# Optimization experiments

Measured on AMD Instinct MI355X. Metric: run time of the kernel, lower is better.

Reference implementation:

```python
import jax, jax.numpy as jnp
import numpy as np
import math

B, S, D, DC, H, L = 8, 4096, 1024, 1024, 16, 2
TOPK, TEMP, MAX_DEPTH, EPS = 2, 1.0, 32, 1e-5

def _gelu(x):
    return jax.nn.gelu(x, approximate=False)

def _ln(x, g=None, b=None):
    mu = x.mean(-1, keepdims=True)
    xc = x - mu
    var = (xc * xc).mean(-1, keepdims=True)
    y = xc * jax.lax.rsqrt(var + EPS)
    if g is not None:
        y = y * g + b
    return y

def setup_inputs() -> dict:
    key = jax.random.key(0)
    ks = iter(jax.random.split(key, 40))
    w = lambda *sh: jax.random.normal(next(ks), sh, dtype=jnp.float32) * 0.02
    inp = {}
    inp['X'] = jax.random.normal(next(ks), (B, S, D), dtype=jnp.float32)
    inp['z'] = jax.random.normal(next(ks), (B, DC), dtype=jnp.float32)
    inp['step_idx'] = 3
    # pool LayerNorm (affine) + input projection
    inp['g_pool'] = jnp.ones((D,)); inp['b_pool'] = jnp.zeros((D,))
    inp['W_inp'] = w(D, DC); inp['b_inp'] = jnp.zeros((DC,))
    # timestep embedding MLP
    inp['Wt1'] = w(DC, 4 * DC); inp['bt1'] = jnp.zeros((4 * DC,))
    inp['Wt2'] = w(4 * DC, DC); inp['bt2'] = jnp.zeros((DC,))
    # cond fusion
    inp['Wc1'] = w(2 * DC, DC); inp['bc1'] = jnp.zeros((DC,))
    inp['Wc2'] = w(DC, DC); inp['bc2'] = jnp.zeros((DC,))
    # denoise blocks (stacked over L)
    inp['W_mod'] = w(L, DC, 4 * DC); inp['b_mod'] = jnp.zeros((L, 4 * DC))
    inp['Wm1'] = w(L, DC, 4 * DC); inp['bm1'] = jnp.zeros((L, 4 * DC))
    inp['Wm2'] = w(L, 4 * DC, DC); inp['bm2'] = jnp.zeros((L, DC))
    # final proj + ln_z
    inp['Wf'] = w(DC, DC); inp['bf'] = jnp.zeros((DC,))
    inp['gz'] = jnp.ones((DC,)); inp['bz'] = jnp.zeros((DC,))
    # router: LN(D+DC) -> Linear -> GELU -> Linear(H)
    inp['gr'] = jnp.ones((D + DC,)); inp['br'] = jnp.zeros((D + DC,))
    inp['Wr1'] = w(D + DC, DC); inp['br1'] = jnp.zeros((DC,))
    inp['Wr2'] = w(DC, H); inp['br2'] = jnp.zeros((H,))
    return inp

def _forward(X, z, step_idx, g_pool, b_pool, W_inp, b_inp, Wt1, bt1, Wt2, bt2,
             Wc1, bc1, Wc2, bc2, W_mod, b_mod, Wm1, bm1, Wm2, bm2,
             Wf, bf, gz, bz, gr, br, Wr1, br1, Wr2, br2):
    # pool tokens -> control vector
    g = _ln(X, g_pool, b_pool).mean(axis=1)            # [B, D]
    x_ctrl = g @ W_inp + b_inp                          # [B, DC]
    # cosine noise schedule, sigma at this depth step
    t = jnp.linspace(0.0, 1.0, MAX_DEPTH)
    sigma_sched = jnp.clip(jnp.cos(t * (math.pi / 2)), 1e-4, None)
    sig = sigma_sched[min(int(step_idx), MAX_DEPTH - 1)]
    # sinusoidal timestep embedding + MLP
    half = DC // 2
    freqs = jnp.exp(-math.log(10000.0) * jnp.arange(half, dtype=jnp.float32) / half)
    args = jnp.broadcast_to(sig * freqs, (B, half))
    emb = jnp.concatenate([jnp.cos(args), jnp.sin(args)], axis=-1)  # [B, DC]
    t_embed = _gelu(emb @ Wt1 + bt1) @ Wt2 + bt2
    # conditioning fusion
    cond = jnp.concatenate([x_ctrl, t_embed], axis=-1)
    cond = _gelu(cond @ Wc1 + bc1) @ Wc2 + bc2          # [B, DC]
    # adaLN denoise blocks
    z_cur = z
    for l in range(L):
        mod = _gelu(cond) @ W_mod[l] + b_mod[l]
        s1, sh1, s2, sh2 = jnp.split(mod, 4, axis=-1)
        h = _ln(z_cur) * (1.0 + s1) + sh1
        h = _gelu(h @ Wm1[l] + bm1[l]) @ Wm2[l] + bm2[l]
        h = h * (1.0 + s2) + sh2
        z_cur = z_cur + h
    z_cur = z_cur @ Wf + bf
    z_cur = _ln(z_cur, gz, bz)                          # [B, DC]
    # token-conditioned router
    zt = jnp.broadcast_to(z_cur[:, None, :], (B, S, DC))
    r = _ln(jnp.concatenate([X, zt], axis=-1), gr, br)  # [B, S, D+DC]
    logits = _gelu(r @ Wr1 + br1) @ Wr2 + br2           # [B, S, H]
    alpha = jax.nn.softmax(logits / TEMP, axis=-1)
    # top-k mask + renormalize
    topv, topi = jax.lax.top_k(alpha, TOPK)
    bi = jnp.arange(B)[:, None, None]
    si = jnp.arange(S)[None, :, None]
    masked = jnp.zeros_like(alpha).at[bi, si, topi].set(topv)
    denom = jnp.maximum(masked.sum(axis=-1, keepdims=True), 1e-12)
    return masked / denom                               # [B, S, H]

def reference(X, z, step_idx, g_pool, b_pool, W_inp, b_inp, Wt1, bt1, Wt2, bt2,
              Wc1, bc1, Wc2, bc2, W_mod, b_mod, Wm1, bm1, Wm2, bm2,
              Wf, bf, gz, bz, gr, br, Wr1, br1, Wr2, br2):
    return _forward(X, z, step_idx, g_pool, b_pool, W_inp, b_inp, Wt1, bt1, Wt2, bt2,
                    Wc1, bc1, Wc2, bc2, W_mod, b_mod, Wm1, bm1, Wm2, bm2,
                    Wf, bf, gz, bz, gr, br, Wr1, br1, Wr2, br2)
```

## Files before the change

kernel.cpp:

```cpp
#include <hip/hip_runtime.h>
#include <cstdint>
#include <cstddef>
#include <math.h>

#define DEV __device__ __forceinline__


typedef short s8v __attribute__((ext_vector_type(8)));
typedef float f4v __attribute__((ext_vector_type(4)));

DEV float geluf(float x) { return 0.5f * x * (1.0f + erff(x * 0.70710678118654752440f)); }
DEV double gelud(double x) { return 0.5 * x * (1.0 + erf(x * 0.70710678118654752440)); }
DEV unsigned short f2us(float f) {
    unsigned u = __float_as_uint(f);
    u += 0x7fffu + ((u >> 16) & 1u);
    return (unsigned short)(u >> 16);
}

DEV void gload16(const void* g, void* l) {
    __builtin_amdgcn_global_load_lds(
        (const __attribute__((address_space(1))) void*)g,
        (__attribute__((address_space(3))) void*)l, 16, 0, 0);
}

DEV void blockReduce2d(double& a, double& b, double* lds ) {
    __syncthreads();
#pragma unroll
    for (int off = 32; off >= 1; off >>= 1) {
        a += __shfl_xor(a, off, 64);
        b += __shfl_xor(b, off, 64);
    }
    int w = threadIdx.x >> 6;
    if ((threadIdx.x & 63) == 0) { lds[w] = a; lds[4 + w] = b; }
    __syncthreads();
    a = lds[0] + lds[1] + lds[2] + lds[3];
    b = lds[4] + lds[5] + lds[6] + lds[7];
    __syncthreads();
}

__global__ __launch_bounds__(256) void pool_kernel(
    const float* __restrict__ X, double* __restrict__ Macc,
    double* __restrict__ tokstats)
{
    int b = blockIdx.y;
    int w = threadIdx.x >> 6, l = threadIdx.x & 63;
    int s0 = blockIdx.x * 64 + w * 16;
    double acc[16];
#pragma unroll
    for (int e = 0; e < 16; e++) acc[e] = 0.0;
    __shared__ double red[4][1024];

    for (int t = 0; t < 16; t++) {
        int s = s0 + t;
        const float* row = X + (size_t)(b * 4096 + s) * 1024;
        float xv[16];
#pragma unroll
        for (int m = 0; m < 16; m++) xv[m] = row[l + 64 * m];
        double s1 = 0.0, s2 = 0.0;
#pragma unroll
        for (int m = 0; m < 16; m++) { double x = (double)xv[m]; s1 += x; s2 += x * x; }
#pragma unroll
        for (int off = 32; off >= 1; off >>= 1) {
            s1 += __shfl_xor(s1, off, 64);
            s2 += __shfl_xor(s2, off, 64);
        }
        double mu = s1 * (1.0 / 1024.0);
        double var = s2 * (1.0 / 1024.0) - mu * mu;
        double istd = 1.0 / sqrt(var + 1e-5);
        if (l == 0) {
            tokstats[(size_t)(b * 4096 + s) * 2]     = s1;
            tokstats[(size_t)(b * 4096 + s) * 2 + 1] = s2;
        }
#pragma unroll
        for (int m = 0; m < 16; m++) acc[m] += ((double)xv[m] - mu) * istd;
    }
#pragma unroll
    for (int m = 0; m < 16; m++) red[w][l + 64 * m] = acc[m];
    __syncthreads();
    for (int d = threadIdx.x; d < 1024; d += 256)
        atomicAdd(&Macc[b * 1024 + d], red[0][d] + red[1][d] + red[2][d] + red[3][d]);
}

__global__ void prep_kernel(const int* __restrict__ step_idx,
                            const float* __restrict__ z,
                            double* __restrict__ emb, double* __restrict__ z0)
{
    int step = step_idx[0];
    if (step > 31) step = 31;
    double t = (double)step / 31.0;
    double sig = cos(t * 1.5707963267948966);
    if (sig < 1e-4) sig = 1e-4;
    for (int k = threadIdx.x; k < 512; k += 256) {
        double fr = exp(-9.210340371976184 * ((double)k / 512.0));
        double a = sig * fr;
        emb[k] = cos(a);
        emb[512 + k] = sin(a);
    }
    for (int i = threadIdx.x; i < 8192; i += 256) z0[i] = (double)z[i];
}

__global__ __launch_bounds__(256) void prepw_kernel(
    const float* __restrict__ Wr1, const float* __restrict__ gr,
    unsigned short* __restrict__ WThi, unsigned short* __restrict__ WTlo)
{
    __shared__ unsigned short th[64][65], tl[64][65];
    int tx = threadIdx.x & 63, ty = threadIdx.x >> 6;
    int i0 = blockIdx.y * 64, j0 = blockIdx.x * 64;
#pragma unroll 4
    for (int k = 0; k < 16; k++) {
        int row = ty * 16 + k;
        float w = (float)((double)gr[i0 + row] * (double)Wr1[(size_t)(i0 + row) * 1024 + j0 + tx]);
        unsigned short hi = f2us(w);
        float hif = __uint_as_float((unsigned)hi << 16);
        unsigned short lo = f2us(w - hif);
        th[row][tx] = hi;
        tl[row][tx] = lo;
    }
    __syncthreads();
#pragma unroll 4
    for (int k = 0; k < 16; k++) {
        int row = ty * 16 + k;
        WThi[(size_t)(j0 + row) * 1024 + i0 + tx] = th[tx][row];
        WTlo[(size_t)(j0 + row) * 1024 + i0 + tx] = tl[tx][row];
    }
}

__global__ __launch_bounds__(256) void colsum_kernel(
    const float* __restrict__ Wr1, const float* __restrict__ gr,
    const float* __restrict__ br, const float* __restrict__ br1,
    double* __restrict__ Cvec, double* __restrict__ hbvec)
{
    int j = blockIdx.x * 256 + threadIdx.x;
    double c = 0.0, bw = 0.0;
    for (int i = 0; i < 2048; i++) {
        double wv = (double)Wr1[(size_t)i * 1024 + j];
        c += (double)gr[i] * wv;
        bw += (double)br[i] * wv;
    }
    Cvec[j] = c;
    hbvec[j] = bw + (double)br1[j];
}

template <int IN, int R>
__global__ __launch_bounds__(256) void gemvd_kernel(
    const float* __restrict__ W, int K, int N, int kchunk, int kstr,
    const double* __restrict__ in0, const double* __restrict__ in1,
    const double* __restrict__ in2,
    const float* __restrict__ ba0, const float* __restrict__ ba1,
    double* __restrict__ out)
{
    const int CH = 64;
    __shared__ double xin[R][CH];
    int tid = threadIdx.x;
    int j = blockIdx.x * 256 + tid;
    int kbeg = blockIdx.y * kchunk;
    double acc[R];
#pragma unroll
    for (int r = 0; r < R; r++) acc[r] = 0.0;

    for (int k0 = kbeg; k0 < kbeg + kchunk; k0 += CH) {
        for (int idx = tid; idx < R * CH; idx += 256) {
            int r = idx / CH, ii = idx % CH, i = k0 + ii;
            double v;
            if (IN == 0) {
                v = in0[(size_t)r * kstr + i] + (ba0 ? (double)ba0[i] : 0.0);
            } else if (IN == 1) {
                v = (double)ba0[i] * (in0[(size_t)r * kstr + i] * (1.0 / 4096.0)) + (double)ba1[i];
            } else if (IN == 2) {
                v = gelud(in0[(size_t)r * kstr + i] + (ba0 ? (double)ba0[i] : 0.0));
            } else if (IN == 3) {
                double mu = in1[r * 2], istd = in1[r * 2 + 1];
                double s1 = in2[(size_t)r * 4096 + i] + (double)ba0[i];
                double sh1 = in2[(size_t)r * 4096 + 1024 + i] + (double)ba0[1024 + i];
                v = (in0[(size_t)r * 1024 + i] - mu) * istd * (1.0 + s1) + sh1;
            } else {
                v = (i < 1024) ? (in0[(size_t)r * 1024 + i] + (double)ba0[i])
                               : (in1[i - 1024] + (double)ba1[i - 1024]);
            }
            xin[r][ii] = v;
        }
        __syncthreads();
#pragma unroll 16
        for (int kk = 0; kk < CH; kk++) {
            double wv = (double)W[(size_t)(k0 + kk) * N + j];
#pragma unroll
            for (int r = 0; r < R; r++) acc[r] += xin[r][kk] * wv;
        }
        __syncthreads();
    }
#pragma unroll
    for (int r = 0; r < R; r++) atomicAdd(&out[(size_t)r * N + j], acc[r]);
}

__global__ void stats8_kernel(const double* __restrict__ z, double* __restrict__ zstats)
{
    __shared__ double lds[8];
    int r = blockIdx.x, tid = threadIdx.x;
    double s = 0.0, ss = 0.0;
    for (int i = tid; i < 1024; i += 256) {
        double v = z[(size_t)r * 1024 + i];
        s += v; ss += v * v;
    }
    blockReduce2d(s, ss, lds);
    if (tid == 0) {
        double mu = s * (1.0 / 1024.0);
        double var = ss * (1.0 / 1024.0) - mu * mu;
        zstats[r * 2] = mu;
        zstats[r * 2 + 1] = 1.0 / sqrt(var + 1e-5);
    }
}

__global__ void resid_kernel(const double* __restrict__ zc, const double* __restrict__ h2pre,
                             const float* __restrict__ bm2,
                             const double* __restrict__ modpre,
                             const float* __restrict__ bmod,
                             double* __restrict__ znew, double* __restrict__ zstats)
{
    __shared__ double lds[8];
    int r = blockIdx.x, tid = threadIdx.x;
    double s = 0.0, ss = 0.0;
#pragma unroll
    for (int c = 0; c < 4; c++) {
        int i = tid + c * 256;
        double s2 = modpre[(size_t)r * 4096 + 2048 + i] + (double)bmod[2048 + i];
        double sh2 = modpre[(size_t)r * 4096 + 3072 + i] + (double)bmod[3072 + i];
        double h = h2pre[(size_t)r * 1024 + i] + (double)bm2[i];
        double v = zc[(size_t)r * 1024 + i] + h * (1.0 + s2) + sh2;
        znew[(size_t)r * 1024 + i] = v;
        s += v; ss += v * v;
    }
    blockReduce2d(s, ss, lds);
    if (tid == 0) {
        double mu = s * (1.0 / 1024.0);
        double var = ss * (1.0 / 1024.0) - mu * mu;
        zstats[r * 2] = mu;
        zstats[r * 2 + 1] = 1.0 / sqrt(var + 1e-5);
    }
}

__global__ void zfinal_kernel(const double* __restrict__ zfpre,
                              const float* __restrict__ bfb,
                              const float* __restrict__ gz,
                              const float* __restrict__ bz,
                              const float* __restrict__ gr,
                              double* __restrict__ zv, double* __restrict__ zrstats)
{
    __shared__ double xb[1024];
    __shared__ double lds[8];
    int r = blockIdx.x, tid = threadIdx.x;
    double s = 0.0, ss = 0.0;
#pragma unroll
    for (int c = 0; c < 4; c++) {
        int i = tid + c * 256;
        double x = zfpre[(size_t)r * 1024 + i] + (double)bfb[i];
        xb[i] = x;
        s += x; ss += x * x;
    }
    blockReduce2d(s, ss, lds);
    double mu = s * (1.0 / 1024.0);
    double var = ss * (1.0 / 1024.0) - mu * mu;
    double istd = 1.0 / sqrt(var + 1e-5);
    double s2 = 0.0, s2s = 0.0;
#pragma unroll
    for (int c = 0; c < 4; c++) {
        int i = tid + c * 256;
        double zf = (xb[i] - mu) * istd * (double)gz[i] + (double)bz[i];
        zv[(size_t)r * 1024 + i] = zf * (double)gr[1024 + i];
        s2 += zf; s2s += zf * zf;
    }
    blockReduce2d(s2, s2s, lds);
    if (tid == 0) { zrstats[r * 2] = s2; zrstats[r * 2 + 1] = s2s; }
}

__global__ __launch_bounds__(256) void router_kernel(
    const float* __restrict__ X, const unsigned short* __restrict__ WThi,
    const unsigned short* __restrict__ WTlo,
    const double* __restrict__ tokstats, const double* __restrict__ zrstats,
    const double* __restrict__ Vmat, const double* __restrict__ Cvec,
    const double* __restrict__ hbvec, const float* __restrict__ Wr2,
    float* __restrict__ logits)
{
    __shared__ struct {
        union {
            struct { float Af[128 * 32]; unsigned short Bh[128 * 32]; unsigned short Bl[128 * 32]; } g;
            struct { float Ht[64 * 133]; float W2[1024]; } e;
        } u;
        float mus[128], iss[128], Vs[128], Cs[128], hbs[128];
    } sm;

    const int tid = threadIdx.x;
    const int n0 = blockIdx.x * 128, tok0 = blockIdx.y * 128;
    const int b = tok0 >> 12;

    if (tid < 128) {
        int tok = tok0 + tid;
        double mu = (tokstats[(size_t)tok * 2] + zrstats[b * 2]) * (1.0 / 2048.0);
        double var = (tokstats[(size_t)tok * 2 + 1] + zrstats[b * 2 + 1]) * (1.0 / 2048.0) - mu * mu;
        sm.mus[tid] = (float)mu;
        sm.iss[tid] = (float)(1.0 / sqrt(var + 1e-5));
    } else {
        int n = tid - 128;
        sm.Vs[n] = (float)Vmat[(size_t)b * 1024 + n0 + n];
        sm.Cs[n] = (float)Cvec[n0 + n];
        sm.hbs[n] = (float)hbvec[n0 + n];
    }

    const int l = tid & 63, wid = tid >> 6;
    const int wm = wid >> 1, wn = wid & 1;
    const int lr = l & 15, q = l >> 4;

    const float* gA[4]; char* lA[4];
#pragma unroll
    for (int it = 0; it < 4; it++) {
        int c = it * 256 + tid;
        int m = c >> 3;
        int pg = (c & 7) ^ (m & 7);
        gA[it] = X + (size_t)(tok0 + m) * 1024 + pg * 4;
        lA[it] = (char*)sm.u.g.Af + c * 16;
    }
    const unsigned short *gBh[2], *gBl[2];
    char *lBh[2], *lBl[2];
#pragma unroll
    for (int it = 0; it < 2; it++) {
        int c = it * 256 + tid;
        int m = c >> 2;
        int p = (c & 3) ^ ((m >> 1) & 3);
        gBh[it] = WThi + (size_t)(n0 + m) * 1024 + p * 8;
        gBl[it] = WTlo + (size_t)(n0 + m) * 1024 + p * 8;
        lBh[it] = (char*)sm.u.g.Bh + c * 16;
        lBl[it] = (char*)sm.u.g.Bl + c * 16;
    }

    int boff[4], aoffr[4], s7a[4];
#pragma unroll
    for (int i = 0; i < 4; i++) {
        int rb = wn * 64 + i * 16 + lr;
        boff[i] = rb * 32 + ((q ^ ((rb >> 1) & 3)) << 3);
        int ra = wm * 64 + i * 16 + lr;
        aoffr[i] = ra * 32;
        s7a[i] = ra & 7;
    }

    f4v acc[4][4];
#pragma unroll
    for (int mi = 0; mi < 4; mi++)
#pragma unroll
        for (int ni = 0; ni < 4; ni++) acc[mi][ni] = (f4v){0.f, 0.f, 0.f, 0.f};

    for (int k0 = 0; k0 < 1024; k0 += 32) {
#pragma unroll
        for (int it = 0; it < 4; it++) gload16(gA[it] + k0, lA[it]);
#pragma unroll
        for (int it = 0; it < 2; it++) {
            gload16(gBh[it] + k0, lBh[it]);
            gload16(gBl[it] + k0, lBl[it]);
        }
        __syncthreads();

        s8v ah[4], al[4], bh4[4], bl4[4];
#pragma unroll
        for (int i = 0; i < 4; i++) {
            const float* Ab = sm.u.g.Af + aoffr[i];
            float4 f0 = *(const float4*)(Ab + ((((2 * q))     ^ s7a[i]) << 2));
            float4 f1 = *(const float4*)(Ab + ((((2 * q) | 1) ^ s7a[i]) << 2));
            unsigned u0 = __float_as_uint(f0.x), u1 = __float_as_uint(f0.y),
                     u2 = __float_as_uint(f0.z), u3 = __float_as_uint(f0.w),
                     u4 = __float_as_uint(f1.x), u5 = __float_as_uint(f1.y),
                     u6 = __float_as_uint(f1.z), u7 = __float_as_uint(f1.w);
            int4 hi4, lo4;
            hi4.x = (int)((u0 >> 16) | (u1 & 0xffff0000u));
            hi4.y = (int)((u2 >> 16) | (u3 & 0xffff0000u));
            hi4.z = (int)((u4 >> 16) | (u5 & 0xffff0000u));
            hi4.w = (int)((u6 >> 16) | (u7 & 0xffff0000u));
            float r0 = f0.x - __uint_as_float(u0 & 0xffff0000u);
            float r1 = f0.y - __uint_as_float(u1 & 0xffff0000u);
            float r2 = f0.z - __uint_as_float(u2 & 0xffff0000u);
            float r3 = f0.w - __uint_as_float(u3 & 0xffff0000u);
            float r4 = f1.x - __uint_as_float(u4 & 0xffff0000u);
            float r5 = f1.y - __uint_as_float(u5 & 0xffff0000u);
            float r6 = f1.z - __uint_as_float(u6 & 0xffff0000u);
            float r7 = f1.w - __uint_as_float(u7 & 0xffff0000u);
            lo4.x = (int)((__float_as_uint(r0) >> 16) | (__float_as_uint(r1) & 0xffff0000u));
            lo4.y = (int)((__float_as_uint(r2) >> 16) | (__float_as_uint(r3) & 0xffff0000u));
            lo4.z = (int)((__float_as_uint(r4) >> 16) | (__float_as_uint(r5) & 0xffff0000u));
            lo4.w = (int)((__float_as_uint(r6) >> 16) | (__float_as_uint(r7) & 0xffff0000u));
            ah[i] = __builtin_bit_cast(s8v, hi4);
            al[i] = __builtin_bit_cast(s8v, lo4);
            bh4[i] = *(const s8v*)(sm.u.g.Bh + boff[i]);
            bl4[i] = *(const s8v*)(sm.u.g.Bl + boff[i]);
        }
#pragma unroll
        for (int mi = 0; mi < 4; mi++)
#pragma unroll
            for (int ni = 0; ni < 4; ni++) {
                acc[mi][ni] = __builtin_amdgcn_mfma_f32_16x16x32_bf16(ah[mi], bh4[ni], acc[mi][ni], 0, 0, 0);
                acc[mi][ni] = __builtin_amdgcn_mfma_f32_16x16x32_bf16(al[mi], bh4[ni], acc[mi][ni], 0, 0, 0);
                acc[mi][ni] = __builtin_amdgcn_mfma_f32_16x16x32_bf16(ah[mi], bl4[ni], acc[mi][ni], 0, 0, 0);
            }
        __syncthreads();
    }

    float lacc[8];
#pragma unroll
    for (int h = 0; h < 8; h++) lacc[h] = 0.f;
    const int g2 = tid >> 7, mrow = tid & 127;

#pragma unroll
    for (int p = 0; p < 2; p++) {
#pragma unroll
        for (int nh = 0; nh < 2; nh++) {
            int ni = 2 * p + nh;
            int n = wn * 64 + ni * 16 + lr;
            int jl = wn * 32 + nh * 16 + lr;
            float Vn = sm.Vs[n], Cn = sm.Cs[n], hbn = sm.hbs[n];
#pragma unroll
            for (int mi = 0; mi < 4; mi++) {
#pragma unroll
                for (int rr = 0; rr < 4; rr++) {
                    int m = wm * 64 + mi * 16 + q * 4 + rr;
                    float h = sm.iss[m] * (acc[mi][ni][rr] + Vn - sm.mus[m] * Cn) + hbn;
                    sm.u.e.Ht[jl * 133 + m] = geluf(h);
                }
            }
        }
        for (int idx = tid; idx < 1024; idx += 256) {
            int jl = idx >> 4;
            int n = ((jl >> 5) << 6) + p * 32 + (jl & 31);
            sm.u.e.W2[idx] = Wr2[(size_t)(n0 + n) * 16 + (idx & 15)];
        }
        __syncthreads();
#pragma unroll 8
        for (int jl = 0; jl < 64; jl++) {
            float x = sm.u.e.Ht[jl * 133 + mrow];
#pragma unroll
            for (int h = 0; h < 8; h++) lacc[h] += x * sm.u.e.W2[jl * 16 + g2 * 8 + h];
        }
        __syncthreads();
    }
#pragma unroll
    for (int h = 0; h < 8; h++)
        atomicAdd(&logits[(size_t)(tok0 + mrow) * 16 + g2 * 8 + h], lacc[h]);
}

#define FLAG_CAP 16384
__global__ __launch_bounds__(256) void softflag_kernel(
    const float* __restrict__ logits, const float* __restrict__ br2,
    float* __restrict__ out, int* __restrict__ cnt, int* __restrict__ flagged)
{
    int t = blockIdx.x * 256 + threadIdx.x;
    float v[16];
    const float4* lp = (const float4*)(logits + (size_t)t * 16);
    float4 a0 = lp[0], a1 = lp[1], a2 = lp[2], a3 = lp[3];
    v[0] = a0.x; v[1] = a0.y; v[2] = a0.z; v[3] = a0.w;
    v[4] = a1.x; v[5] = a1.y; v[6] = a1.z; v[7] = a1.w;
    v[8] = a2.x; v[9] = a2.y; v[10] = a2.z; v[11] = a2.w;
    v[12] = a3.x; v[13] = a3.y; v[14] = a3.z; v[15] = a3.w;
#pragma unroll
    for (int h = 0; h < 16; h++) v[h] += br2[h];
    int i1 = 0; float b1 = v[0];
#pragma unroll
    for (int h = 1; h < 16; h++) if (v[h] > b1) { b1 = v[h]; i1 = h; }
    int i2 = -1; float b2 = -3.4e38f;
#pragma unroll
    for (int h = 0; h < 16; h++) if (h != i1 && v[h] > b2) { b2 = v[h]; i2 = h; }
    float b3 = -3.4e38f;
#pragma unroll
    for (int h = 0; h < 16; h++) if (h != i1 && h != i2 && v[h] > b3) b3 = v[h];
    float mx = b1;
    float e1 = expf(b1 - mx), e2 = expf(b2 - mx);
    float s = 0.f;
#pragma unroll
    for (int h = 0; h < 16; h++) s += expf(v[h] - mx);
    float a1v = e1 / s, a2v = e2 / s;
    float den = fmaxf(a1v + a2v, 1e-12f);
    float r1 = a1v / den, r2 = a2v / den;
    float o[16];
#pragma unroll
    for (int h = 0; h < 16; h++) o[h] = (h == i1 ? r1 : (h == i2 ? r2 : 0.f));
    float4* op = (float4*)(out + (size_t)t * 16);
    op[0] = make_float4(o[0], o[1], o[2], o[3]);
    op[1] = make_float4(o[4], o[5], o[6], o[7]);
    op[2] = make_float4(o[8], o[9], o[10], o[11]);
    op[3] = make_float4(o[12], o[13], o[14], o[15]);
    if (b2 - b3 < 1e-3f) {
        int slot = atomicAdd(cnt, 1);
        if (slot < FLAG_CAP) flagged[slot] = t;
    }
}

__global__ void flagstat_kernel(const float* __restrict__ X,
                                const double* __restrict__ zrstats,
                                const int* __restrict__ cnt,
                                const int* __restrict__ flagged,
                                double* __restrict__ fstats)
{
    int n = cnt[0]; if (n > FLAG_CAP) n = FLAG_CAP;
    int s = blockIdx.x;
    if (s >= n) return;
    int tok = flagged[s], b = tok >> 12;
    int l = threadIdx.x;
    double s1 = 0.0, s2 = 0.0;
#pragma unroll
    for (int m = 0; m < 16; m++) {
        double x = (double)X[(size_t)tok * 1024 + l + 64 * m];
        s1 += x; s2 += x * x;
    }
#pragma unroll
    for (int off = 32; off >= 1; off >>= 1) {
        s1 += __shfl_xor(s1, off, 64);
        s2 += __shfl_xor(s2, off, 64);
    }
    if (l == 0) {
        double mu = (s1 + zrstats[b * 2]) * (1.0 / 2048.0);
        double var = (s2 + zrstats[b * 2 + 1]) * (1.0 / 2048.0) - mu * mu;
        fstats[s * 2] = mu;
        fstats[s * 2 + 1] = 1.0 / sqrt(var + 1e-5);
    }
}

__global__ __launch_bounds__(256) void exact2_kernel(
    const float* __restrict__ X, const float* __restrict__ Wr1,
    const float* __restrict__ gr, const double* __restrict__ zv,
    const double* __restrict__ Cvec, const double* __restrict__ hbvec,
    const float* __restrict__ Wr2,
    const int* __restrict__ cnt, const int* __restrict__ flagged,
    const double* __restrict__ fstats, double* __restrict__ exlog)
{
    int n = cnt[0]; if (n > FLAG_CAP) n = FLAG_CAP;
    const int c = blockIdx.y;
    if (c * 16 >= n) return;
    int nt = n - c * 16; if (nt > 16) nt = 16;

    __shared__ double aS[16][65];
    __shared__ double gS[16][129];
    __shared__ double mus[16], iss[16];
    __shared__ int toks[16];

    const int tid = threadIdx.x;
    const int j0 = blockIdx.x * 128;
    const int jl = tid & 127;
    const int j = j0 + jl;
    const int tg = (tid >> 7) * 8;

    if (tid < 16) {
        if (tid < nt) {
            toks[tid] = flagged[c * 16 + tid];
            mus[tid] = fstats[(size_t)(c * 16 + tid) * 2];
            iss[tid] = fstats[(size_t)(c * 16 + tid) * 2 + 1];
        } else {
            toks[tid] = 0; mus[tid] = 0.0; iss[tid] = 0.0;
        }
    }
    __syncthreads();

    double acc[8];
#pragma unroll
    for (int t = 0; t < 8; t++) acc[t] = 0.0;

    for (int i0 = 0; i0 < 2048; i0 += 64) {
        for (int idx = tid; idx < 1024; idx += 256) {
            int t = idx >> 6, ii = idx & 63, i = i0 + ii;
            double v = 0.0;
            if (t < nt) {
                int tok = toks[t];
                if (i < 1024)
                    v = (double)X[(size_t)tok * 1024 + i] * (double)gr[i];
                else
                    v = zv[(size_t)(tok >> 12) * 1024 + (i - 1024)];
            }
            aS[t][ii] = v;
        }
        __syncthreads();
#pragma unroll 8
        for (int ii = 0; ii < 64; ii++) {
            double wv = (double)Wr1[(size_t)(i0 + ii) * 1024 + j];
#pragma unroll
            for (int t = 0; t < 8; t++) acc[t] += aS[tg + t][ii] * wv;
        }
        __syncthreads();
    }

    {
        double Cj = Cvec[j], hbj = hbvec[j];
#pragma unroll
        for (int t = 0; t < 8; t++) {
            double pre = iss[tg + t] * (acc[t] - mus[tg + t] * Cj) + hbj;
            gS[tg + t][jl] = gelud(pre);
        }
    }
    __syncthreads();

    {
        int t = tid >> 4, h = tid & 15;
        double p = 0.0;
#pragma unroll 8
        for (int j2 = 0; j2 < 128; j2++)
            p += gS[t][j2] * (double)Wr2[(size_t)(j0 + j2) * 16 + h];
        if (t < nt)
            atomicAdd(&exlog[(size_t)(c * 16 + t) * 16 + h], p);
    }
}

__global__ __launch_bounds__(256) void fix_kernel(
    const double* __restrict__ exlog, const float* __restrict__ br2,
    const int* __restrict__ cnt, const int* __restrict__ flagged,
    float* __restrict__ out)
{
    int s = blockIdx.x * 256 + threadIdx.x;
    int n = cnt[0]; if (n > FLAG_CAP) n = FLAG_CAP;
    if (s >= n) return;
    int tok = flagged[s];
    double v[16];
#pragma unroll
    for (int h = 0; h < 16; h++) v[h] = exlog[(size_t)s * 16 + h] + (double)br2[h];
    int i1 = 0; double b1 = v[0];
#pragma unroll
    for (int h = 1; h < 16; h++) if (v[h] > b1) { b1 = v[h]; i1 = h; }
    int i2 = -1; double b2 = -1e300;
#pragma unroll
    for (int h = 0; h < 16; h++) if (h != i1 && v[h] > b2) { b2 = v[h]; i2 = h; }
    double ssum = 0.0;
#pragma unroll
    for (int h = 0; h < 16; h++) ssum += exp(v[h] - b1);
    double a1v = exp(b1 - b1) / ssum, a2v = exp(b2 - b1) / ssum;
    double den = a1v + a2v; if (den < 1e-12) den = 1e-12;
    float r1 = (float)(a1v / den), r2 = (float)(a2v / den);
#pragma unroll
    for (int h = 0; h < 16; h++)
        out[(size_t)tok * 16 + h] = (h == i1 ? r1 : (h == i2 ? r2 : 0.f));
}

extern "C" void kernel_launch(void* const* d_in, const int* in_sizes, int n_in,
                              void* d_out, int out_size, void* d_ws, size_t ws_size,
                              hipStream_t stream)
{
    const float* X      = (const float*)d_in[0];
    const float* z_in   = (const float*)d_in[1];
    const int*   stepi  = (const int*)d_in[2];
    const float* g_pool = (const float*)d_in[3];
    const float* b_pool = (const float*)d_in[4];
    const float* W_inp  = (const float*)d_in[5];
    const float* b_inp  = (const float*)d_in[6];
    const float* Wt1    = (const float*)d_in[7];
    const float* bt1    = (const float*)d_in[8];
    const float* Wt2    = (const float*)d_in[9];
    const float* bt2    = (const float*)d_in[10];
    const float* Wc1    = (const float*)d_in[11];
    const float* bc1    = (const float*)d_in[12];
    const float* Wc2    = (const float*)d_in[13];
    const float* bc2    = (const float*)d_in[14];
    const float* W_mod  = (const float*)d_in[15];
    const float* b_mod  = (const float*)d_in[16];
    const float* Wm1    = (const float*)d_in[17];
    const float* bm1    = (const float*)d_in[18];
    const float* Wm2    = (const float*)d_in[19];
    const float* bm2    = (const float*)d_in[20];
    const float* Wf     = (const float*)d_in[21];
    const float* bf_b   = (const float*)d_in[22];
    const float* gz     = (const float*)d_in[23];
    const float* bz     = (const float*)d_in[24];
    const float* gr     = (const float*)d_in[25];
    const float* br     = (const float*)d_in[26];
    const float* Wr1    = (const float*)d_in[27];
    const float* br1    = (const float*)d_in[28];
    const float* Wr2    = (const float*)d_in[29];
    const float* br2    = (const float*)d_in[30];

    char* wsb = (char*)d_ws;
    const size_t OB_LOGA  = 0;
    const size_t OB_EXLOG = 2097152;
    const size_t OB_CNT   = 4194304;
    const size_t OB_FLAG  = 4194368;
    const size_t OB_MACC  = 4259904;
    const size_t OB_XCTRL = 4325440;
    const size_t OB_TH1   = 4390976;
    const size_t OB_TEMB  = 4423744;
    const size_t OB_CH    = 4431936;
    const size_t OB_COND  = 4497472;
    const size_t OB_MOD   = 4563008;
    const size_t OB_H1    = 5087296;
    const size_t OB_H2    = 5611584;
    const size_t OB_ZFPRE = 5742656;
    const size_t OB_V     = 5808192;
    const size_t ZEND     = 5873728;
    const size_t OB_TOKST = 5873728;
    const size_t OB_FSTAT = 6398016;
    const size_t OB_EMB   = 6660160;
    const size_t OB_ZB0   = 6668352;
    const size_t OB_ZB1   = 6733888;
    const size_t OB_ZST   = 6799424;
    const size_t OB_ZRST  = 6799552;
    const size_t OB_ZV    = 6799680;
    const size_t OB_CVEC  = 6865216;
    const size_t OB_HB    = 6873408;
    const size_t OB_WTHI  = 6881600;
    const size_t OB_WTLO  = 8978752;

    unsigned short* WThi = (unsigned short*)(wsb + OB_WTHI);
    unsigned short* WTlo = (unsigned short*)(wsb + OB_WTLO);
    int* cntp  = (int*)(wsb + OB_CNT);
    int* flagp = (int*)(wsb + OB_FLAG);

    hipMemsetAsync(d_ws, 0, ZEND, stream);

    pool_kernel<<<dim3(64, 8), 256, 0, stream>>>(X, (double*)(wsb + OB_MACC), (double*)(wsb + OB_TOKST));
    prep_kernel<<<1, 256, 0, stream>>>(stepi, z_in, (double*)(wsb + OB_EMB), (double*)(wsb + OB_ZB0));
    prepw_kernel<<<dim3(16, 16), 256, 0, stream>>>(Wr1, gr, WThi, WTlo);
    colsum_kernel<<<4, 256, 0, stream>>>(Wr1, gr, br, br1, (double*)(wsb + OB_CVEC), (double*)(wsb + OB_HB));

    gemvd_kernel<1, 8><<<dim3(4, 16), 256, 0, stream>>>(W_inp, 1024, 1024, 64, 1024,
        (double*)(wsb + OB_MACC), nullptr, nullptr, g_pool, b_pool, (double*)(wsb + OB_XCTRL));
    gemvd_kernel<0, 1><<<dim3(16, 16), 256, 0, stream>>>(Wt1, 1024, 4096, 64, 1024,
        (double*)(wsb + OB_EMB), nullptr, nullptr, nullptr, nullptr, (double*)(wsb + OB_TH1));
    gemvd_kernel<2, 1><<<dim3(4, 16), 256, 0, stream>>>(Wt2, 4096, 1024, 256, 4096,
        (double*)(wsb + OB_TH1), nullptr, nullptr, bt1, nullptr, (double*)(wsb + OB_TEMB));
    gemvd_kernel<4, 8><<<dim3(4, 16), 256, 0, stream>>>(Wc1, 2048, 1024, 128, 1024,
        (double*)(wsb + OB_XCTRL), (double*)(wsb + OB_TEMB), nullptr, b_inp, bt2, (double*)(wsb + OB_CH));
    gemvd_kernel<2, 8><<<dim3(4, 16), 256, 0, stream>>>(Wc2, 1024, 1024, 64, 1024,
        (double*)(wsb + OB_CH), nullptr, nullptr, bc1, nullptr, (double*)(wsb + OB_COND));

    stats8_kernel<<<8, 256, 0, stream>>>((double*)(wsb + OB_ZB0), (double*)(wsb + OB_ZST));

    for (int ll = 0; ll < 2; ll++) {
        double* zcur  = (double*)(wsb + (ll == 0 ? OB_ZB0 : OB_ZB1));
        double* znext = (double*)(wsb + (ll == 0 ? OB_ZB1 : OB_ZB0));
        double* modp  = (double*)(wsb + OB_MOD) + (size_t)ll * 32768;
        double* h1p   = (double*)(wsb + OB_H1) + (size_t)ll * 32768;
        double* h2p   = (double*)(wsb + OB_H2) + (size_t)ll * 8192;
        gemvd_kernel<2, 8><<<dim3(16, 16), 256, 0, stream>>>(W_mod + (size_t)ll * 4194304,
            1024, 4096, 64, 1024, (double*)(wsb + OB_COND), nullptr, nullptr, bc2, nullptr, modp);
        gemvd_kernel<3, 8><<<dim3(16, 16), 256, 0, stream>>>(Wm1 + (size_t)ll * 4194304,
            1024, 4096, 64, 1024, zcur, (double*)(wsb + OB_ZST), modp, b_mod + ll * 4096, nullptr, h1p);
        gemvd_kernel<2, 8><<<dim3(4, 16), 256, 0, stream>>>(Wm2 + (size_t)ll * 4194304,
            4096, 1024, 256, 4096, h1p, nullptr, nullptr, bm1 + ll * 4096, nullptr, h2p);
        resid_kernel<<<8, 256, 0, stream>>>(zcur, h2p, bm2 + ll * 1024, modp,
                                            b_mod + ll * 4096, znext, (double*)(wsb + OB_ZST));
    }

    gemvd_kernel<0, 8><<<dim3(4, 16), 256, 0, stream>>>(Wf, 1024, 1024, 64, 1024,
        (double*)(wsb + OB_ZB0), nullptr, nullptr, nullptr, nullptr, (double*)(wsb + OB_ZFPRE));
    zfinal_kernel<<<8, 256, 0, stream>>>((double*)(wsb + OB_ZFPRE), bf_b, gz, bz, gr,
                                         (double*)(wsb + OB_ZV), (double*)(wsb + OB_ZRST));
    gemvd_kernel<0, 8><<<dim3(4, 16), 256, 0, stream>>>(Wr1 + (size_t)1024 * 1024,
        1024, 1024, 64, 1024, (double*)(wsb + OB_ZV), nullptr, nullptr, nullptr, nullptr,
        (double*)(wsb + OB_V));

    router_kernel<<<dim3(8, 256), 256, 0, stream>>>(X, WThi, WTlo,
        (double*)(wsb + OB_TOKST), (double*)(wsb + OB_ZRST), (double*)(wsb + OB_V),
        (double*)(wsb + OB_CVEC), (double*)(wsb + OB_HB), Wr2, (float*)(wsb + OB_LOGA));

    softflag_kernel<<<128, 256, 0, stream>>>((float*)(wsb + OB_LOGA), br2,
        (float*)d_out, cntp, flagp);
    flagstat_kernel<<<16384, 64, 0, stream>>>(X, (double*)(wsb + OB_ZRST), cntp, flagp,
        (double*)(wsb + OB_FSTAT));
    exact2_kernel<<<dim3(8, 1024), 256, 0, stream>>>(X, Wr1, gr, (double*)(wsb + OB_ZV),
        (double*)(wsb + OB_CVEC), (double*)(wsb + OB_HB), Wr2, cntp, flagp,
        (double*)(wsb + OB_FSTAT), (double*)(wsb + OB_EXLOG));
    fix_kernel<<<64, 256, 0, stream>>>((double*)(wsb + OB_EXLOG), br2, cntp, flagp,
        (float*)d_out);
}
```

Before: 1.810 ms.

## Pre-split X into bf16 hi/lo in pool pass and add MFMA router2 kernel

Measured after the change: 1.729 ms. -4.5%, faster.

```diff
diff --git a/kernel.cpp b/kernel.cpp
--- a/kernel.cpp
+++ b/kernel.cpp
@@ -40,7 +40,8 @@
 
 __global__ __launch_bounds__(256) void pool_kernel(
     const float* __restrict__ X, double* __restrict__ Macc,
-    double* __restrict__ tokstats)
+    double* __restrict__ tokstats,
+    unsigned short* __restrict__ XH, unsigned short* __restrict__ XL)
 {
     int b = blockIdx.y;
     int w = threadIdx.x >> 6, l = threadIdx.x & 63;
@@ -56,6 +57,16 @@
         float xv[16];
 #pragma unroll
         for (int m = 0; m < 16; m++) xv[m] = row[l + 64 * m];
+        if (XH) {
+            size_t base = (size_t)(b * 4096 + s) * 1024 + l;
+#pragma unroll
+            for (int m = 0; m < 16; m++) {
+                unsigned u = __float_as_uint(xv[m]);
+                XH[base + 64 * m] = (unsigned short)(u >> 16);
+                float r = xv[m] - __uint_as_float(u & 0xffff0000u);
+                XL[base + 64 * m] = (unsigned short)(__float_as_uint(r) >> 16);
+            }
+        }
         double s1 = 0.0, s2 = 0.0;
 #pragma unroll
         for (int m = 0; m < 16; m++) { double x = (double)xv[m]; s1 += x; s2 += x * x; }
@@ -131,14 +142,18 @@
     double* __restrict__ Cvec, double* __restrict__ hbvec)
 {
     int j = blockIdx.x * 256 + threadIdx.x;
+    int i0 = blockIdx.y * 128;
     double c = 0.0, bw = 0.0;
-    for (int i = 0; i < 2048; i++) {
+#pragma unroll 4
+    for (int k = 0; k < 128; k++) {
+        int i = i0 + k;
         double wv = (double)Wr1[(size_t)i * 1024 + j];
         c += (double)gr[i] * wv;
         bw += (double)br[i] * wv;
     }
-    Cvec[j] = c;
-    hbvec[j] = bw + (double)br1[j];
+    if (blockIdx.y == 0) bw += (double)br1[j];
+    atomicAdd(&Cvec[j], c);
+    atomicAdd(&hbvec[j], bw);
 }
 
 template <int IN, int R>
@@ -270,6 +285,147 @@
     }
     blockReduce2d(s2, s2s, lds);
     if (tid == 0) { zrstats[r * 2] = s2; zrstats[r * 2 + 1] = s2s; }
+}
+
+__global__ __launch_bounds__(256) void router2_kernel(
+    const unsigned short* __restrict__ XH, const unsigned short* __restrict__ XL,
+    const unsigned short* __restrict__ WThi, const unsigned short* __restrict__ WTlo,
+    const double* __restrict__ tokstats, const double* __restrict__ zrstats,
+    const double* __restrict__ Vmat, const double* __restrict__ Cvec,
+    const double* __restrict__ hbvec, const float* __restrict__ Wr2,
+    float* __restrict__ logits)
+{
+    __shared__ struct {
+        union {
+            struct { unsigned short Ah[128 * 32], Al[128 * 32],
+                                    Bh[128 * 32], Bl[128 * 32]; } g;
+            struct { float Ht[64 * 133]; float W2[1024]; } e;
+        } u;
+        float mus[128], iss[128], Vs[128], Cs[128], hbs[128];
+    } sm;
+
+    const int tid = threadIdx.x;
+    const int id = blockIdx.x;
+    const int xcd = id & 7, local = id >> 3;
+    const int tokTile = xcd * 32 + (local >> 3);
+    const int nTile = local & 7;
+    const int n0 = nTile * 128, tok0 = tokTile * 128;
+    const int b = tok0 >> 12;
+
+    if (tid < 128) {
+        int tok = tok0 + tid;
+        double mu = (tokstats[(size_t)tok * 2] + zrstats[b * 2]) * (1.0 / 2048.0);
+        double var = (tokstats[(size_t)tok * 2 + 1] + zrstats[b * 2 + 1]) * (1.0 / 2048.0) - mu * mu;
+        sm.mus[tid] = (float)mu;
+        sm.iss[tid] = (float)(1.0 / sqrt(var + 1e-5));
+    } else {
+        int n = tid - 128;
+        sm.Vs[n] = (float)Vmat[(size_t)b * 1024 + n0 + n];
+        sm.Cs[n] = (float)Cvec[n0 + n];
+        sm.hbs[n] = (float)hbvec[n0 + n];
+    }
+
+    const int l = tid & 63, wid = tid >> 6;
+    const int wm = wid >> 1, wn = wid & 1;
+    const int lr = l & 15, q = l >> 4;
+
+    const unsigned short* gS[8]; char* lS[8];
+    {
+        const unsigned short* srcs[4] = {
+            XH + (size_t)tok0 * 1024, XL + (size_t)tok0 * 1024,
+            WThi + (size_t)n0 * 1024, WTlo + (size_t)n0 * 1024 };
+        char* dsts[4] = { (char*)sm.u.g.Ah, (char*)sm.u.g.Al,
+                          (char*)sm.u.g.Bh, (char*)sm.u.g.Bl };
+#pragma unroll
+        for (int s = 0; s < 4; s++)
+#pragma unroll
+            for (int it = 0; it < 2; it++) {
+                int c = it * 256 + tid;
+                int m = c >> 2, p = (c & 3) ^ ((m >> 1) & 3);
+                gS[s * 2 + it] = srcs[s] + (size_t)m * 1024 + p * 8;
+                lS[s * 2 + it] = dsts[s] + c * 16;
+            }
+    }
+
+    int aoff[4], boff[4];
+#pragma unroll
+    for (int i = 0; i < 4; i++) {
+        int ra = wm * 64 + i * 16 + lr;
+        aoff[i] = ra * 32 + ((q ^ ((ra >> 1) & 3)) << 3);
+        int rb = wn * 64 + i * 16 + lr;
+        boff[i] = rb * 32 + ((q ^ ((rb >> 1) & 3)) << 3);
+    }
+
+    f4v acc[4][4];
+#pragma unroll
+    for (int mi = 0; mi < 4; mi++)
+#pragma unroll
+        for (int ni = 0; ni < 4; ni++) acc[mi][ni] = (f4v){0.f, 0.f, 0.f, 0.f};
+
+    for (int k0 = 0; k0 < 1024; k0 += 32) {
+#pragma unroll
+        for (int t = 0; t < 8; t++) gload16(gS[t] + k0, lS[t]);
+        __syncthreads();
+
+        s8v ah[4], al[4], bh4[4], bl4[4];
+#pragma unroll
+        for (int i = 0; i < 4; i++) {
+            ah[i]  = *(const s8v*)(sm.u.g.Ah + aoff[i]);
+            al[i]  = *(const s8v*)(sm.u.g.Al + aoff[i]);
+            bh4[i] = *(const s8v*)(sm.u.g.Bh + boff[i]);
+            bl4[i] = *(const s8v*)(sm.u.g.Bl + boff[i]);
+        }
+#pragma unroll
+        for (int mi = 0; mi < 4; mi++)
+#pragma unroll
+            for (int ni = 0; ni < 4; ni++) {
+                acc[mi][ni] = __builtin_amdgcn_mfma_f32_16x16x32_bf16(ah[mi], bh4[ni], acc[mi][ni], 0, 0, 0);
+                acc[mi][ni] = __builtin_amdgcn_mfma_f32_16x16x32_bf16(al[mi], bh4[ni], acc[mi][ni], 0, 0, 0);
+                acc[mi][ni] = __builtin_amdgcn_mfma_f32_16x16x32_bf16(ah[mi], bl4[ni], acc[mi][ni], 0, 0, 0);
+            }
+        __syncthreads();
+    }
+
+    float lacc[8];
+#pragma unroll
+    for (int h = 0; h < 8; h++) lacc[h] = 0.f;
+    const int g2 = tid >> 7, mrow = tid & 127;
+
+#pragma unroll
+    for (int p = 0; p < 2; p++) {
+#pragma unroll
+        for (int nh = 0; nh < 2; nh++) {
+            int ni = 2 * p + nh;
+            int n = wn * 64 + ni * 16 + lr;
+            int jl = wn * 32 + nh * 16 + lr;
+            float Vn = sm.Vs[n], Cn = sm.Cs[n], hbn = sm.hbs[n];
+#pragma unroll
+            for (int mi = 0; mi < 4; mi++) {
+#pragma unroll
+                for (int rr = 0; rr < 4; rr++) {
+                    int m = wm * 64 + mi * 16 + q * 4 + rr;
+                    float h = sm.iss[m] * (acc[mi][ni][rr] + Vn - sm.mus[m] * Cn) + hbn;
+                    sm.u.e.Ht[jl * 133 + m] = geluf(h);
+                }
+            }
+        }
+        for (int idx = tid; idx < 1024; idx += 256) {
+            int jl = idx >> 4;
+            int n = ((jl >> 5) << 6) + p * 32 + (jl & 31);
+            sm.u.e.W2[idx] = Wr2[(size_t)(n0 + n) * 16 + (idx & 15)];
+        }
+        __syncthreads();
+#pragma unroll 8
+        for (int jl = 0; jl < 64; jl++) {
+            float x = sm.u.e.Ht[jl * 133 + mrow];
+#pragma unroll
+            for (int h = 0; h < 8; h++) lacc[h] += x * sm.u.e.W2[jl * 16 + g2 * 8 + h];
+        }
+        __syncthreads();
+    }
+#pragma unroll
+    for (int h = 0; h < 8; h++)
+        atomicAdd(&logits[(size_t)(tok0 + mrow) * 16 + g2 * 8 + h], lacc[h]);
 }
 
 __global__ __launch_bounds__(256) void router_kernel(
@@ -682,7 +838,6 @@
     const size_t OB_H2    = 5611584;
     const size_t OB_ZFPRE = 5742656;
     const size_t OB_V     = 5808192;
-    const size_t ZEND     = 5873728;
     const size_t OB_TOKST = 5873728;
     const size_t OB_FSTAT = 6398016;
     const size_t OB_EMB   = 6660160;
@@ -693,20 +848,30 @@
     const size_t OB_ZV    = 6799680;
     const size_t OB_CVEC  = 6865216;
     const size_t OB_HB    = 6873408;
+    const size_t ZEND     = 6881600;
     const size_t OB_WTHI  = 6881600;
     const size_t OB_WTLO  = 8978752;
+    const size_t OB_XH    = 11075904;
+    const size_t OB_XL    = 78184768;
+    const size_t WS_BIG   = 145293632;
 
     unsigned short* WThi = (unsigned short*)(wsb + OB_WTHI);
     unsigned short* WTlo = (unsigned short*)(wsb + OB_WTLO);
     int* cntp  = (int*)(wsb + OB_CNT);
     int* flagp = (int*)(wsb + OB_FLAG);
 
+    const bool big = ws_size >= WS_BIG;
+    unsigned short* XHp = big ? (unsigned short*)(wsb + OB_XH) : nullptr;
+    unsigned short* XLp = big ? (unsigned short*)(wsb + OB_XL) : nullptr;
+
     hipMemsetAsync(d_ws, 0, ZEND, stream);
 
-    pool_kernel<<<dim3(64, 8), 256, 0, stream>>>(X, (double*)(wsb + OB_MACC), (double*)(wsb + OB_TOKST));
+    pool_kernel<<<dim3(64, 8), 256, 0, stream>>>(X, (double*)(wsb + OB_MACC),
+                                                 (double*)(wsb + OB_TOKST), XHp, XLp);
     prep_kernel<<<1, 256, 0, stream>>>(stepi, z_in, (double*)(wsb + OB_EMB), (double*)(wsb + OB_ZB0));
     prepw_kernel<<<dim3(16, 16), 256, 0, stream>>>(Wr1, gr, WThi, WTlo);
-    colsum_kernel<<<4, 256, 0, stream>>>(Wr1, gr, br, br1, (double*)(wsb + OB_CVEC), (double*)(wsb + OB_HB));
+    colsum_kernel<<<dim3(4, 16), 256, 0, stream>>>(Wr1, gr, br, br1,
+        (double*)(wsb + OB_CVEC), (double*)(wsb + OB_HB));
 
     gemvd_kernel<1, 8><<<dim3(4, 16), 256, 0, stream>>>(W_inp, 1024, 1024, 64, 1024,
         (double*)(wsb + OB_MACC), nullptr, nullptr, g_pool, b_pool, (double*)(wsb + OB_XCTRL));
@@ -745,9 +910,15 @@
         1024, 1024, 64, 1024, (double*)(wsb + OB_ZV), nullptr, nullptr, nullptr, nullptr,
         (double*)(wsb + OB_V));
 
-    router_kernel<<<dim3(8, 256), 256, 0, stream>>>(X, WThi, WTlo,
-        (double*)(wsb + OB_TOKST), (double*)(wsb + OB_ZRST), (double*)(wsb + OB_V),
-        (double*)(wsb + OB_CVEC), (double*)(wsb + OB_HB), Wr2, (float*)(wsb + OB_LOGA));
+    if (big) {
+        router2_kernel<<<2048, 256, 0, stream>>>(XHp, XLp, WThi, WTlo,
+            (double*)(wsb + OB_TOKST), (double*)(wsb + OB_ZRST), (double*)(wsb + OB_V),
+            (double*)(wsb + OB_CVEC), (double*)(wsb + OB_HB), Wr2, (float*)(wsb + OB_LOGA));
+    } else {
+        router_kernel<<<dim3(8, 256), 256, 0, stream>>>(X, WThi, WTlo,
+            (double*)(wsb + OB_TOKST), (double*)(wsb + OB_ZRST), (double*)(wsb + OB_V),
+            (double*)(wsb + OB_CVEC), (double*)(wsb + OB_HB), Wr2, (float*)(wsb + OB_LOGA));
+    }
 
     softflag_kernel<<<128, 256, 0, stream>>>((float*)(wsb + OB_LOGA), br2,
         (float*)d_out, cntp, flagp);
```
